# Performance work log

Hardware: AMD Instinct MI355X
Metric: run time of the kernel (lower is better)

The kernel has to match this reference:

```python
import jax, jax.numpy as jnp
import numpy as np
import math

D_MODEL = 1024
HEADS = 16
D_K = D_MODEL // HEADS
NUM_TURNS = 30
VOCAB_B = NUM_TURNS ** 2  # 900


def setup_inputs() -> dict:
    key = jax.random.key(0)
    ks = jax.random.split(key, 16)
    bs, Lq, Lk = 4, 512, 2048
    q = jax.random.normal(ks[0], (bs, Lq, D_MODEL), jnp.float32)
    k = jax.random.normal(ks[1], (bs, Lk, D_MODEL), jnp.float32)
    v = jax.random.normal(ks[2], (bs, Lk, D_MODEL), jnp.float32)
    b_idx = jax.random.randint(ks[3], (bs, Lq, Lk), 0, VOCAB_B, jnp.int32)
    mask = jax.random.randint(ks[4], (bs, Lq, Lk), 0, 2, jnp.int32)
    s = 1.0 / math.sqrt(D_MODEL)
    Wq = jax.random.normal(ks[5], (D_MODEL, D_MODEL), jnp.float32) * s
    bq = jnp.zeros((D_MODEL,), jnp.float32)
    Wk = jax.random.normal(ks[6], (D_MODEL, D_MODEL), jnp.float32) * s
    bk = jnp.zeros((D_MODEL,), jnp.float32)
    Wv = jax.random.normal(ks[7], (D_MODEL, D_MODEL), jnp.float32) * s
    bv = jnp.zeros((D_MODEL,), jnp.float32)
    Wo = jax.random.normal(ks[8], (D_MODEL, D_MODEL), jnp.float32) * s
    bo = jnp.zeros((D_MODEL,), jnp.float32)
    # bias embedding table, padding_idx=0 -> zero row
    b_table = jax.random.normal(ks[9], (VOCAB_B, HEADS), jnp.float32) * 0.02
    b_table = b_table.at[0].set(0.0)
    return {"q": q, "k": k, "v": v, "b_idx": b_idx, "mask": mask,
            "Wq": Wq, "bq": bq, "Wk": Wk, "bk": bk, "Wv": Wv, "bv": bv,
            "Wo": Wo, "bo": bo, "b_table": b_table}


def reference(q, k, v, b_idx, mask, Wq, bq, Wk, bk, Wv, bv, Wo, bo, b_table):
    bs, Lq, _ = q.shape
    Lk = k.shape[1]
    # projections, reshape to (bs, h, L, d_k)
    qh = (q @ Wq.T + bq).reshape(bs, Lq, HEADS, D_K).transpose(0, 2, 1, 3)
    kh = (k @ Wk.T + bk).reshape(bs, Lk, HEADS, D_K).transpose(0, 2, 1, 3)
    vh = (v @ Wv.T + bv).reshape(bs, Lk, HEADS, D_K).transpose(0, 2, 1, 3)
    # learned additive bias: embedding lookup (bs,Lq,Lk,h) -> (bs,h,Lq,Lk)
    b = b_table[b_idx].transpose(0, 3, 1, 2)
    scores = jnp.einsum('bhqd,bhkd->bhqk', qh, kh) / math.sqrt(D_K) + b
    scores = jnp.where(mask[:, None] == 0, jnp.float32(-1e9), scores)
    attn = jax.nn.softmax(scores, axis=-1)
    out = jnp.einsum('bhqk,bhkd->bhqd', attn, vh)
    out = out.transpose(0, 2, 1, 3).reshape(bs, Lq, D_MODEL)
    return out @ Wo.T + bo
```

## Files before the change

### kernel.cpp

```cpp
#include <hip/hip_runtime.h>
#include <hip/hip_bf16.h>

#define H 16
#define DK 64
#define DM 1024
#define LQ 512
#define LK 2048
#define BSZ 4

typedef __hip_bfloat16 bf16;
typedef __attribute__((ext_vector_type(8))) short short8;
typedef __attribute__((ext_vector_type(4))) short short4v;
typedef __attribute__((ext_vector_type(4))) float f32x4;


__global__ __launch_bounds__(256) void fused_cvt(
    const float* __restrict__ q, const float* __restrict__ k, const float* __restrict__ v,
    const int* __restrict__ bidx, const int* __restrict__ msk,
    const float* __restrict__ Wq, const float* __restrict__ Wk,
    const float* __restrict__ Wv, const float* __restrict__ Wo,
    const float* __restrict__ btab,
    bf16* __restrict__ qb, bf16* __restrict__ kb, bf16* __restrict__ vb,
    bf16* __restrict__ Wqb, bf16* __restrict__ Wkb, bf16* __restrict__ Wvb,
    bf16* __restrict__ Wob, short* __restrict__ pkd, float* __restrict__ btabT) {
  const int blk = blockIdx.x, tid = threadIdx.x;
  const float* src;
  bf16* dst;
  int base;
  if (blk < 2048)       { src = q;  dst = qb;  base = blk; }
  else if (blk < 10240) { src = k;  dst = kb;  base = blk - 2048; }
  else if (blk < 18432) { src = v;  dst = vb;  base = blk - 10240; }
  else if (blk < 19456) { src = Wq; dst = Wqb; base = blk - 18432; }
  else if (blk < 20480) { src = Wk; dst = Wkb; base = blk - 19456; }
  else if (blk < 21504) { src = Wv; dst = Wvb; base = blk - 20480; }
  else if (blk < 22528) { src = Wo; dst = Wob; base = blk - 21504; }
  else if (blk < 26624) {
    int i = (blk - 22528) * 1024 + tid * 4;
    int4 a = *reinterpret_cast<const int4*>(bidx + i);
    int4 m = *reinterpret_cast<const int4*>(msk + i);
    short4 r;
    r.x = m.x ? (short)a.x : (short)-1;
    r.y = m.y ? (short)a.y : (short)-1;
    r.z = m.z ? (short)a.z : (short)-1;
    r.w = m.w ? (short)a.w : (short)-1;
    *reinterpret_cast<short4*>(pkd + i) = r;
    return;
  } else {
    for (int j = tid; j < 900 * H; j += 256) {
      int hh = j / 900, i = j - hh * 900;
      btabT[hh * 900 + i] = btab[i * H + hh] - 10.0f;
    }
    return;
  }
  int i = base * 1024 + tid * 4;
  float4 val = *reinterpret_cast<const float4*>(src + i);
  bf16 o0 = __float2bfloat16(val.x), o1 = __float2bfloat16(val.y);
  bf16 o2 = __float2bfloat16(val.z), o3 = __float2bfloat16(val.w);
  short4 pk;
  pk.x = *reinterpret_cast<short*>(&o0);
  pk.y = *reinterpret_cast<short*>(&o1);
  pk.z = *reinterpret_cast<short*>(&o2);
  pk.w = *reinterpret_cast<short*>(&o3);
  *reinterpret_cast<short4*>(reinterpret_cast<short*>(dst) + i) = pk;
}


__device__ __forceinline__ void g2lds16(const bf16* g, bf16* l) {
  __builtin_amdgcn_global_load_lds(
      (__attribute__((address_space(1))) void*)(g),
      (__attribute__((address_space(3))) void*)(l), 16, 0, 0);
}

template <int MODE, int TM>
__global__ __launch_bounds__(256) void gemm_bt(const bf16* __restrict__ A,
                                               const bf16* __restrict__ B,
                                               const float* __restrict__ bias,
                                               void* __restrict__ out,
                                               int M, int N, int K, int Lrows) {
  __shared__ bf16 As[TM * 32];
  __shared__ bf16 Bs[128 * 32];
  constexpr int NT = (TM == 128) ? 4 : 2;
  const int tid = threadIdx.x;
  const int wave = tid >> 6, lane = tid & 63;
  const int quad = lane >> 4, l15 = lane & 15;
  const int rowbase = (TM == 128) ? (wave >> 1) * 64 : 0;
  const int colbase = (TM == 128) ? (wave & 1) * 64 : wave * 32;
  const int rowA0 = blockIdx.x * TM, colB0 = blockIdx.y * 128;
  const int srow = lane >> 2, skq = lane & 3;

  f32x4 acc[4][NT];
  const f32x4 zero = {0.f, 0.f, 0.f, 0.f};
  for (int mt = 0; mt < 4; mt++)
    for (int nt = 0; nt < NT; nt++) acc[mt][nt] = zero;

  for (int k0 = 0; k0 < K; k0 += 32) {
    if (TM == 128) {
      for (int c = 0; c < 2; ++c) {
        int r = wave * 32 + c * 16;
        g2lds16(A + (size_t)(rowA0 + r + srow) * K + k0 + skq * 8, As + r * 32);
      }
    } else {
      int r = wave * 16;
      g2lds16(A + (size_t)(rowA0 + r + srow) * K + k0 + skq * 8, As + r * 32);
    }
    for (int c = 0; c < 2; ++c) {
      int r = wave * 32 + c * 16;
      g2lds16(B + (size_t)(colB0 + r + srow) * K + k0 + skq * 8, Bs + r * 32);
    }
    __syncthreads();
    short8 af[4], bfr[NT];
    for (int mt = 0; mt < 4; mt++)
      af[mt] = *reinterpret_cast<const short8*>(As + (rowbase + mt * 16 + l15) * 32 + quad * 8);
    for (int nt = 0; nt < NT; nt++)
      bfr[nt] = *reinterpret_cast<const short8*>(Bs + (colbase + nt * 16 + l15) * 32 + quad * 8);
    for (int mt = 0; mt < 4; mt++)
      for (int nt = 0; nt < NT; nt++) {
        if (MODE == 1)
          acc[mt][nt] = __builtin_amdgcn_mfma_f32_16x16x32_bf16(bfr[nt], af[mt], acc[mt][nt], 0, 0, 0);
        else
          acc[mt][nt] = __builtin_amdgcn_mfma_f32_16x16x32_bf16(af[mt], bfr[nt], acc[mt][nt], 0, 0, 0);
      }
    __syncthreads();
  }

  const int bb = (MODE == 2) ? 0 : (rowA0 / Lrows);
  const int lb = (MODE == 2) ? rowA0 : (rowA0 - bb * Lrows);
  if (MODE == 1) {
    for (int mt = 0; mt < 4; mt++) {
      int key = lb + rowbase + mt * 16 + l15;
      for (int nt = 0; nt < NT; nt++) {
        f32x4 v = acc[mt][nt];
        for (int r = 0; r < 4; r++) {
          int ncol = colB0 + colbase + nt * 16 + quad * 4 + r;
          float bv = bias[ncol];
          int hh = ncol >> 6, d = ncol & 63;
          ((bf16*)out)[((size_t)((bb * H + hh) * DK + d)) * LK + key] =
              __float2bfloat16(v[r] + bv);
        }
      }
    }
    return;
  }
  for (int nt = 0; nt < NT; nt++) {
    int col = colB0 + colbase + nt * 16 + l15;
    float bv = bias[col];
    int hh = col >> 6, d = col & 63;
    for (int mt = 0; mt < 4; mt++) {
      int lrow0 = lb + rowbase + mt * 16 + quad * 4;
      f32x4 v = acc[mt][nt];
      for (int r = 0; r < 4; r++) {
        float val = v[r] + bv;
        if (MODE == 0) {
          ((bf16*)out)[(((size_t)(bb * H + hh) * Lrows + lrow0 + r) << 6) + d] = __float2bfloat16(val);
        } else {
          ((float*)out)[(size_t)(lrow0 + r) * N + col] = val;
        }
      }
    }
  }
}


__global__ __launch_bounds__(256) void attn6(const bf16* __restrict__ Qh,
                                             const bf16* __restrict__ Kh,
                                             const bf16* __restrict__ Vt,
                                             const short* __restrict__ pkm,
                                             const float* __restrict__ btabT,
                                             float* __restrict__ Opart,
                                             float* __restrict__ L) {
  __shared__ __align__(16) bf16 Kbuf[2][64 * 64];
  __shared__ __align__(16) bf16 Vbuf[2][64 * 64];
  __shared__ float bts[900];
  const int tid = threadIdx.x;
  const int wave = tid >> 6, lane = tid & 63;
  const int quad = lane >> 4, l15 = lane & 15;
  const int bh = blockIdx.x, b = bh >> 4, h = bh & 15;
  const int qt = blockIdx.y, z = blockIdx.z;
  const int key_base = z * 1024;

  for (int i = tid; i < 900; i += 256) bts[i] = btabT[h * 900 + i];

  const int q = qt * 64 + wave * 16 + l15;
  short8 qf[2];
  for (int ks = 0; ks < 2; ks++)
    qf[ks] = *reinterpret_cast<const short8*>(
        Qh + ((size_t)bh * LQ + q) * DK + ks * 32 + quad * 8);

  const bf16* kbase = Kh + ((size_t)bh * LK + key_base) * DK;
  const bf16* vbase = Vt + ((size_t)bh * DK) * LK + key_base;
  const short* pkrow = pkm + ((size_t)b * LQ + q) * LK + key_base;

  const int srow_off = lane >> 3;
  const int sseg = ((lane & 7) - srow_off) & 7;

  f32x4 of[4];
  float denom = 0.f;
  const f32x4 zero = {0.f, 0.f, 0.f, 0.f};
  for (int dt = 0; dt < 4; dt++) of[dt] = zero;

  for (int c = 0; c < 2; c++) {
    int row = wave * 16 + c * 8 + srow_off;
    g2lds16(kbase + (size_t)row * DK + sseg * 8,
            &Kbuf[0][(wave * 16 + c * 8) * 64]);
    g2lds16(vbase + (size_t)row * LK + sseg * 8,
            &Vbuf[0][(wave * 16 + c * 8) * 64]);
  }
  short4v pkv[4];
  for (int nt = 0; nt < 4; nt++)
    pkv[nt] = *reinterpret_cast<const short4v*>(pkrow + nt * 16 + quad * 4);

  __syncthreads();

  for (int kc = 0; kc < 16; ++kc) {
    const int buf = kc & 1;

    short4v pk_n[4];
    if (kc < 15) {
      const int key1 = (kc + 1) * 64;
      for (int c = 0; c < 2; c++) {
        int row = wave * 16 + c * 8 + srow_off;
        g2lds16(kbase + (size_t)(key1 + row) * DK + sseg * 8,
                &Kbuf[buf ^ 1][(wave * 16 + c * 8) * 64]);
        g2lds16(vbase + (size_t)row * LK + key1 + sseg * 8,
                &Vbuf[buf ^ 1][(wave * 16 + c * 8) * 64]);
      }
      for (int nt = 0; nt < 4; nt++)
        pk_n[nt] = *reinterpret_cast<const short4v*>(pkrow + key1 + nt * 16 + quad * 4);
    }

    f32x4 sa[4];
    for (int nt = 0; nt < 4; nt++) sa[nt] = zero;
    for (int nt = 0; nt < 4; nt++)
      for (int ks = 0; ks < 2; ks++) {
        short8 kf = *reinterpret_cast<const short8*>(
            &Kbuf[buf][(nt * 16 + l15) * 64 + (((ks * 4 + quad + l15) & 7) << 3)]);
        sa[nt] = __builtin_amdgcn_mfma_f32_16x16x32_bf16(kf, qf[ks], sa[nt], 0, 0, 0);
      }

    short4v vf[4][4];
    for (int dt = 0; dt < 4; dt++)
      for (int nt = 0; nt < 4; nt++)
        vf[dt][nt] = *reinterpret_cast<const short4v*>(
            &Vbuf[buf][(dt * 16 + l15) * 64 +
                       (((nt * 2 + (quad >> 1) + l15) & 7) << 3) + ((quad & 1) << 2)]);

    short4v pf[4];
    for (int nt = 0; nt < 4; nt++) {
      float p[4];
      for (int r = 0; r < 4; r++) {
        int pv = pkv[nt][r];
        float t = fmaf(sa[nt][r], 0.125f, bts[pv < 0 ? 0 : pv]);
        t = (pv < 0) ? -1e9f : t;
        p[r] = __expf(t);
      }
      denom += (p[0] + p[1]) + (p[2] + p[3]);
      short4v pk4;
      for (int r = 0; r < 4; r++) {
        bf16 tb = __float2bfloat16(p[r]);
        pk4[r] = *reinterpret_cast<short*>(&tb);
      }
      pf[nt] = pk4;
    }

    for (int dt = 0; dt < 4; dt++)
      for (int nt = 0; nt < 4; nt++)
        of[dt] = __builtin_amdgcn_mfma_f32_16x16x16bf16_1k(vf[dt][nt], pf[nt], of[dt], 0, 0, 0);

    if (kc < 15)
      for (int nt = 0; nt < 4; nt++) pkv[nt] = pk_n[nt];

    __syncthreads();
  }

  denom += __shfl_xor(denom, 16, 64);
  denom += __shfl_xor(denom, 32, 64);

  size_t rowi = ((size_t)z * 64 + bh) * LQ + q;
  float* orow = Opart + rowi * 64;
  for (int dt = 0; dt < 4; dt++)
    *reinterpret_cast<f32x4*>(orow + dt * 16 + quad * 4) = of[dt];
  if (quad == 0) L[rowi] = denom;
}

__global__ __launch_bounds__(256) void attn_combine(const float* __restrict__ Opart,
                                                    const float* __restrict__ L,
                                                    bf16* __restrict__ Ob) {
  int t = blockIdx.x * 256 + threadIdx.x;
  int g = t * 4;
  int row = g >> 6, d0 = g & 63;
  float l = L[row] + L[32768 + row];
  float4 o;
  float4 p0 = *reinterpret_cast<const float4*>(Opart + ((size_t)row << 6) + d0);
  float4 p1 = *reinterpret_cast<const float4*>(Opart + (((size_t)32768 + row) << 6) + d0);
  o.x = p0.x + p1.x; o.y = p0.y + p1.y; o.z = p0.z + p1.z; o.w = p0.w + p1.w;
  float inv = 1.f / l;
  bf16 t0 = __float2bfloat16(o.x * inv), t1 = __float2bfloat16(o.y * inv);
  bf16 t2 = __float2bfloat16(o.z * inv), t3 = __float2bfloat16(o.w * inv);
  short4 pk;
  pk.x = *reinterpret_cast<short*>(&t0);
  pk.y = *reinterpret_cast<short*>(&t1);
  pk.z = *reinterpret_cast<short*>(&t2);
  pk.w = *reinterpret_cast<short*>(&t3);
  int bh = row >> 9, qq = row & 511, b_ = bh >> 4, h = bh & 15;
  *reinterpret_cast<short4*>(Ob + ((size_t)(b_ * LQ + qq)) * DM + h * 64 + d0) = pk;
}


extern "C" void kernel_launch(void* const* d_in, const int* in_sizes, int n_in,
                              void* d_out, int out_size, void* d_ws, size_t ws_size,
                              hipStream_t stream) {
  const float* q = (const float*)d_in[0];
  const float* k = (const float*)d_in[1];
  const float* v = (const float*)d_in[2];
  const int* bidx = (const int*)d_in[3];
  const int* mask = (const int*)d_in[4];
  const float* Wq = (const float*)d_in[5];
  const float* bq = (const float*)d_in[6];
  const float* Wk = (const float*)d_in[7];
  const float* bk = (const float*)d_in[8];
  const float* Wv = (const float*)d_in[9];
  const float* bv = (const float*)d_in[10];
  const float* Wo = (const float*)d_in[11];
  const float* bo = (const float*)d_in[12];
  const float* btab = (const float*)d_in[13];

  char* ws = (char*)d_ws;
  bf16* qb  = (bf16*)(ws + 0);
  bf16* kb  = (bf16*)(ws + 4194304);
  bf16* vb  = (bf16*)(ws + 20971520);
  bf16* Wqb = (bf16*)(ws + 37748736);
  bf16* Wkb = (bf16*)(ws + 39845888);
  bf16* Wvb = (bf16*)(ws + 41943040);
  bf16* Wob = (bf16*)(ws + 44040192);
  bf16* Qh  = (bf16*)(ws + 46137344);
  bf16* Kh  = (bf16*)(ws + 50331648);
  bf16* Vt  = (bf16*)(ws + 67108864);
  short* pkd = (short*)(ws + 83886080);
  bf16* Ob  = (bf16*)(ws + 92274688);
  float* btabT = (float*)(ws + 92274688);
  float* Opart = (float*)(ws + 0);
  float* L     = (float*)(ws + 16777216);
  (void)ws_size; (void)in_sizes; (void)n_in; (void)out_size;

  hipLaunchKernelGGL(fused_cvt, dim3(26625), dim3(256), 0, stream,
                     q, k, v, bidx, mask, Wq, Wk, Wv, Wo, btab,
                     qb, kb, vb, Wqb, Wkb, Wvb, Wob, pkd, btabT);

  hipLaunchKernelGGL((gemm_bt<0, 64>), dim3(32, 8), dim3(256), 0, stream,
                     qb, Wqb, bq, (void*)Qh, 2048, 1024, 1024, LQ);
  hipLaunchKernelGGL((gemm_bt<0, 128>), dim3(64, 8), dim3(256), 0, stream,
                     kb, Wkb, bk, (void*)Kh, 8192, 1024, 1024, LK);
  hipLaunchKernelGGL((gemm_bt<1, 128>), dim3(64, 8), dim3(256), 0, stream,
                     vb, Wvb, bv, (void*)Vt, 8192, 1024, 1024, LK);

  hipLaunchKernelGGL(attn6, dim3(BSZ * H, LQ / 64, 2), dim3(256), 0, stream,
                     Qh, Kh, Vt, pkd, btabT, Opart, L);
  hipLaunchKernelGGL(attn_combine, dim3(2048), dim3(256), 0, stream,
                     Opart, L, Ob);

  hipLaunchKernelGGL((gemm_bt<2, 64>), dim3(32, 8), dim3(256), 0, stream,
                     Ob, Wob, bo, d_out, 2048, 1024, 1024, LQ);
}
```

Before: 342.5 us.

## Merge QKV projections, split attention 4-way over keys, fold mask into bias table

The Q, K and V projection GEMMs are merged into one launch with a flat block index, cutting launch gaps and tail effects. Attention is split into four key chunks of 512 with a swizzled block order and a 6-blocks-per-CU launch bound, and the combine kernel now sums four partials. V is read straight from global memory into registers instead of being staged in LDS, which frees shared memory but adds uncoalesced global loads. The mask is encoded as a sentinel index 900 whose table entry is -1e9, and the table is prescaled by log2(e) so exp2 replaces exp and the per-element mask select disappears.

Result: slower. 469.8 us (+37.2%).

```diff
diff --git a/kernel.cpp b/kernel.cpp
--- a/kernel.cpp
+++ b/kernel.cpp
@@ -12,6 +12,9 @@
 typedef __attribute__((ext_vector_type(8))) short short8;
 typedef __attribute__((ext_vector_type(4))) short short4v;
 typedef __attribute__((ext_vector_type(4))) float f32x4;
+
+#define LOG2E 1.44269504f
+#define SC2 0.18033688f
 
 
 __global__ __launch_bounds__(256) void fused_cvt(
@@ -39,16 +42,16 @@
     int4 a = *reinterpret_cast<const int4*>(bidx + i);
     int4 m = *reinterpret_cast<const int4*>(msk + i);
     short4 r;
-    r.x = m.x ? (short)a.x : (short)-1;
-    r.y = m.y ? (short)a.y : (short)-1;
-    r.z = m.z ? (short)a.z : (short)-1;
-    r.w = m.w ? (short)a.w : (short)-1;
+    r.x = m.x ? (short)a.x : (short)900;
+    r.y = m.y ? (short)a.y : (short)900;
+    r.z = m.z ? (short)a.z : (short)900;
+    r.w = m.w ? (short)a.w : (short)900;
     *reinterpret_cast<short4*>(pkd + i) = r;
     return;
   } else {
-    for (int j = tid; j < 900 * H; j += 256) {
-      int hh = j / 900, i = j - hh * 900;
-      btabT[hh * 900 + i] = btab[i * H + hh] - 10.0f;
+    for (int j = tid; j < H * 901; j += 256) {
+      int hh = j / 901, i = j - hh * 901;
+      btabT[j] = (i == 900) ? -1e9f : (btab[i * H + hh] - 10.0f) * LOG2E;
     }
     return;
   }
@@ -72,20 +75,20 @@
 }
 
 template <int MODE, int TM>
-__global__ __launch_bounds__(256) void gemm_bt(const bf16* __restrict__ A,
-                                               const bf16* __restrict__ B,
-                                               const float* __restrict__ bias,
-                                               void* __restrict__ out,
-                                               int M, int N, int K, int Lrows) {
-  __shared__ bf16 As[TM * 32];
-  __shared__ bf16 Bs[128 * 32];
+__device__ __forceinline__ void gemm_body(bf16* __restrict__ As, bf16* __restrict__ Bs,
+                                          const bf16* __restrict__ A,
+                                          const bf16* __restrict__ B,
+                                          const float* __restrict__ bias,
+                                          void* __restrict__ out,
+                                          int M, int N, int K, int Lrows,
+                                          int bx, int by) {
   constexpr int NT = (TM == 128) ? 4 : 2;
   const int tid = threadIdx.x;
   const int wave = tid >> 6, lane = tid & 63;
   const int quad = lane >> 4, l15 = lane & 15;
   const int rowbase = (TM == 128) ? (wave >> 1) * 64 : 0;
   const int colbase = (TM == 128) ? (wave & 1) * 64 : wave * 32;
-  const int rowA0 = blockIdx.x * TM, colB0 = blockIdx.y * 128;
+  const int rowA0 = bx * TM, colB0 = by * 128;
   const int srow = lane >> 2, skq = lane & 3;
 
   f32x4 acc[4][NT];
@@ -160,25 +163,51 @@
   }
 }
 
-
-__global__ __launch_bounds__(256) void attn6(const bf16* __restrict__ Qh,
-                                             const bf16* __restrict__ Kh,
-                                             const bf16* __restrict__ Vt,
-                                             const short* __restrict__ pkm,
-                                             const float* __restrict__ btabT,
-                                             float* __restrict__ Opart,
-                                             float* __restrict__ L) {
+__global__ __launch_bounds__(256) void proj_qkv(
+    const bf16* __restrict__ kb, const bf16* __restrict__ Wkb, const float* __restrict__ bk, bf16* __restrict__ Kh,
+    const bf16* __restrict__ vb, const bf16* __restrict__ Wvb, const float* __restrict__ bv, bf16* __restrict__ Vt,
+    const bf16* __restrict__ qb, const bf16* __restrict__ Wqb, const float* __restrict__ bq, bf16* __restrict__ Qh) {
+  __shared__ __align__(16) bf16 As[128 * 32];
+  __shared__ __align__(16) bf16 Bs[128 * 32];
+  const int blk = blockIdx.x;
+  if (blk < 512)
+    gemm_body<0, 128>(As, Bs, kb, Wkb, bk, (void*)Kh, 8192, 1024, 1024, LK, blk >> 3, blk & 7);
+  else if (blk < 1024)
+    gemm_body<1, 128>(As, Bs, vb, Wvb, bv, (void*)Vt, 8192, 1024, 1024, LK, (blk - 512) >> 3, (blk - 512) & 7);
+  else
+    gemm_body<0, 64>(As, Bs, qb, Wqb, bq, (void*)Qh, 2048, 1024, 1024, LQ, (blk - 1024) >> 3, (blk - 1024) & 7);
+}
+
+__global__ __launch_bounds__(256) void gemm_o(const bf16* __restrict__ A,
+                                              const bf16* __restrict__ B,
+                                              const float* __restrict__ bias,
+                                              float* __restrict__ out) {
+  __shared__ __align__(16) bf16 As[64 * 32];
+  __shared__ __align__(16) bf16 Bs[128 * 32];
+  gemm_body<2, 64>(As, Bs, A, B, bias, (void*)out, 2048, 1024, 1024, LQ, blockIdx.x, blockIdx.y);
+}
+
+
+__global__ __launch_bounds__(256, 6) void attn7(const bf16* __restrict__ Qh,
+                                                const bf16* __restrict__ Kh,
+                                                const bf16* __restrict__ Vt,
+                                                const short* __restrict__ pkm,
+                                                const float* __restrict__ btabT,
+                                                float* __restrict__ Opart,
+                                                float* __restrict__ L) {
   __shared__ __align__(16) bf16 Kbuf[2][64 * 64];
-  __shared__ __align__(16) bf16 Vbuf[2][64 * 64];
-  __shared__ float bts[900];
+  __shared__ float bts[901];
   const int tid = threadIdx.x;
   const int wave = tid >> 6, lane = tid & 63;
   const int quad = lane >> 4, l15 = lane & 15;
-  const int bh = blockIdx.x, b = bh >> 4, h = bh & 15;
-  const int qt = blockIdx.y, z = blockIdx.z;
-  const int key_base = z * 1024;
-
-  for (int i = tid; i < 900; i += 256) bts[i] = btabT[h * 900 + i];
+  const int lin = blockIdx.x;
+  const int bh = ((lin & 7) << 3) | ((lin >> 3) & 7);
+  const int qt = (lin >> 6) & 7;
+  const int zi = lin >> 9;
+  const int b = bh >> 4, h = bh & 15;
+  const int key_base = zi * 512;
+
+  for (int i = tid; i < 901; i += 256) bts[i] = btabT[h * 901 + i];
 
   const int q = qt * 64 + wave * 16 + l15;
   short8 qf[2];
@@ -200,33 +229,32 @@
 
   for (int c = 0; c < 2; c++) {
     int row = wave * 16 + c * 8 + srow_off;
-    g2lds16(kbase + (size_t)row * DK + sseg * 8,
-            &Kbuf[0][(wave * 16 + c * 8) * 64]);
-    g2lds16(vbase + (size_t)row * LK + sseg * 8,
-            &Vbuf[0][(wave * 16 + c * 8) * 64]);
-  }
-  short4v pkv[4];
-  for (int nt = 0; nt < 4; nt++)
-    pkv[nt] = *reinterpret_cast<const short4v*>(pkrow + nt * 16 + quad * 4);
-
+    g2lds16(kbase + (size_t)row * DK + sseg * 8, &Kbuf[0][(wave * 16 + c * 8) * 64]);
+  }
   __syncthreads();
 
-  for (int kc = 0; kc < 16; ++kc) {
+  for (int kc = 0; kc < 8; ++kc) {
     const int buf = kc & 1;
 
-    short4v pk_n[4];
-    if (kc < 15) {
+    if (kc < 7) {
       const int key1 = (kc + 1) * 64;
       for (int c = 0; c < 2; c++) {
         int row = wave * 16 + c * 8 + srow_off;
         g2lds16(kbase + (size_t)(key1 + row) * DK + sseg * 8,
                 &Kbuf[buf ^ 1][(wave * 16 + c * 8) * 64]);
-        g2lds16(vbase + (size_t)row * LK + key1 + sseg * 8,
-                &Vbuf[buf ^ 1][(wave * 16 + c * 8) * 64]);
-      }
+      }
+    }
+
+    short4v pkv[4];
+    for (int nt = 0; nt < 4; nt++)
+      pkv[nt] = *reinterpret_cast<const short4v*>(pkrow + kc * 64 + nt * 16 + quad * 4);
+
+    const bf16* vch = vbase + kc * 64;
+    short4v vf[4][4];
+    for (int dt = 0; dt < 4; dt++)
       for (int nt = 0; nt < 4; nt++)
-        pk_n[nt] = *reinterpret_cast<const short4v*>(pkrow + key1 + nt * 16 + quad * 4);
-    }
+        vf[dt][nt] = *reinterpret_cast<const short4v*>(
+            vch + (size_t)(dt * 16 + l15) * LK + nt * 16 + quad * 4);
 
     f32x4 sa[4];
     for (int nt = 0; nt < 4; nt++) sa[nt] = zero;
@@ -237,21 +265,12 @@
         sa[nt] = __builtin_amdgcn_mfma_f32_16x16x32_bf16(kf, qf[ks], sa[nt], 0, 0, 0);
       }
 
-    short4v vf[4][4];
-    for (int dt = 0; dt < 4; dt++)
-      for (int nt = 0; nt < 4; nt++)
-        vf[dt][nt] = *reinterpret_cast<const short4v*>(
-            &Vbuf[buf][(dt * 16 + l15) * 64 +
-                       (((nt * 2 + (quad >> 1) + l15) & 7) << 3) + ((quad & 1) << 2)]);
-
     short4v pf[4];
     for (int nt = 0; nt < 4; nt++) {
       float p[4];
       for (int r = 0; r < 4; r++) {
-        int pv = pkv[nt][r];
-        float t = fmaf(sa[nt][r], 0.125f, bts[pv < 0 ? 0 : pv]);
-        t = (pv < 0) ? -1e9f : t;
-        p[r] = __expf(t);
+        float t = fmaf(sa[nt][r], SC2, bts[pkv[nt][r]]);
+        p[r] = __builtin_amdgcn_exp2f(t);
       }
       denom += (p[0] + p[1]) + (p[2] + p[3]);
       short4v pk4;
@@ -266,16 +285,13 @@
       for (int nt = 0; nt < 4; nt++)
         of[dt] = __builtin_amdgcn_mfma_f32_16x16x16bf16_1k(vf[dt][nt], pf[nt], of[dt], 0, 0, 0);
 
-    if (kc < 15)
-      for (int nt = 0; nt < 4; nt++) pkv[nt] = pk_n[nt];
-
-    __syncthreads();
+    if (kc < 7) __syncthreads();
   }
 
   denom += __shfl_xor(denom, 16, 64);
   denom += __shfl_xor(denom, 32, 64);
 
-  size_t rowi = ((size_t)z * 64 + bh) * LQ + q;
+  size_t rowi = ((size_t)zi * 64 + bh) * LQ + q;
   float* orow = Opart + rowi * 64;
   for (int dt = 0; dt < 4; dt++)
     *reinterpret_cast<f32x4*>(orow + dt * 16 + quad * 4) = of[dt];
@@ -288,11 +304,16 @@
   int t = blockIdx.x * 256 + threadIdx.x;
   int g = t * 4;
   int row = g >> 6, d0 = g & 63;
-  float l = L[row] + L[32768 + row];
+  float l = (L[row] + L[32768 + row]) + (L[65536 + row] + L[98304 + row]);
+  float4 p0 = *reinterpret_cast<const float4*>(Opart + ((size_t)row << 6) + d0);
+  float4 p1 = *reinterpret_cast<const float4*>(Opart + (((size_t)row + 32768) << 6) + d0);
+  float4 p2 = *reinterpret_cast<const float4*>(Opart + (((size_t)row + 65536) << 6) + d0);
+  float4 p3 = *reinterpret_cast<const float4*>(Opart + (((size_t)row + 98304) << 6) + d0);
   float4 o;
-  float4 p0 = *reinterpret_cast<const float4*>(Opart + ((size_t)row << 6) + d0);
-  float4 p1 = *reinterpret_cast<const float4*>(Opart + (((size_t)32768 + row) << 6) + d0);
-  o.x = p0.x + p1.x; o.y = p0.y + p1.y; o.z = p0.z + p1.z; o.w = p0.w + p1.w;
+  o.x = (p0.x + p1.x) + (p2.x + p3.x);
+  o.y = (p0.y + p1.y) + (p2.y + p3.y);
+  o.z = (p0.z + p1.z) + (p2.z + p3.z);
+  o.w = (p0.w + p1.w) + (p2.w + p3.w);
   float inv = 1.f / l;
   bf16 t0 = __float2bfloat16(o.x * inv), t1 = __float2bfloat16(o.y * inv);
   bf16 t2 = __float2bfloat16(o.z * inv), t3 = __float2bfloat16(o.w * inv);
@@ -339,25 +360,21 @@
   bf16* Ob  = (bf16*)(ws + 92274688);
   float* btabT = (float*)(ws + 92274688);
   float* Opart = (float*)(ws + 0);
-  float* L     = (float*)(ws + 16777216);
+  float* L     = (float*)(ws + 33554432);
   (void)ws_size; (void)in_sizes; (void)n_in; (void)out_size;
 
   hipLaunchKernelGGL(fused_cvt, dim3(26625), dim3(256), 0, stream,
                      q, k, v, bidx, mask, Wq, Wk, Wv, Wo, btab,
                      qb, kb, vb, Wqb, Wkb, Wvb, Wob, pkd, btabT);
 
-  hipLaunchKernelGGL((gemm_bt<0, 64>), dim3(32, 8), dim3(256), 0, stream,
-                     qb, Wqb, bq, (void*)Qh, 2048, 1024, 1024, LQ);
-  hipLaunchKernelGGL((gemm_bt<0, 128>), dim3(64, 8), dim3(256), 0, stream,
-                     kb, Wkb, bk, (void*)Kh, 8192, 1024, 1024, LK);
-  hipLaunchKernelGGL((gemm_bt<1, 128>), dim3(64, 8), dim3(256), 0, stream,
-                     vb, Wvb, bv, (void*)Vt, 8192, 1024, 1024, LK);
-
-  hipLaunchKernelGGL(attn6, dim3(BSZ * H, LQ / 64, 2), dim3(256), 0, stream,
+  hipLaunchKernelGGL(proj_qkv, dim3(1280), dim3(256), 0, stream,
+                     kb, Wkb, bk, Kh, vb, Wvb, bv, Vt, qb, Wqb, bq, Qh);
+
+  hipLaunchKernelGGL(attn7, dim3(2048), dim3(256), 0, stream,
                      Qh, Kh, Vt, pkd, btabT, Opart, L);
   hipLaunchKernelGGL(attn_combine, dim3(2048), dim3(256), 0, stream,
                      Opart, L, Ob);
 
-  hipLaunchKernelGGL((gemm_bt<2, 64>), dim3(32, 8), dim3(256), 0, stream,
-                     Ob, Wob, bo, d_out, 2048, 1024, 1024, LQ);
-}
+  hipLaunchKernelGGL(gemm_o, dim3(32, 8), dim3(256), 0, stream,
+                     Ob, Wob, bo, (float*)d_out);
+}
```
